# Optimization experiments

Hardware: AMD Instinct MI355X
Metric: run time of the kernel (lower is better)

## Reference

```python
import jax, jax.numpy as jnp
import numpy as np

LEAKY_SLOPE = 0.2  # tf.nn.leaky_relu default alpha
N_NODES = 50000
N_EDGES = 800000
IN_DIM = 128
OUT_DIM = 64
HEADS = 4
MLP_HID = 256
MLP_OUT = 128


def setup_inputs() -> dict:
    key = jax.random.key(0)
    ks = jax.random.split(key, 10)
    node_embeddings = jax.random.normal(ks[0], (N_NODES, IN_DIM), dtype=jnp.float32)
    src = jax.random.randint(ks[1], (N_EDGES,), 0, N_NODES, dtype=jnp.int32)
    dst = jax.random.randint(ks[2], (N_EDGES,), 0, N_NODES, dtype=jnp.int32)
    # glorot-ish scales
    W_n = jax.random.normal(ks[3], (HEADS, IN_DIM, OUT_DIM), dtype=jnp.float32) * (1.0 / np.sqrt(IN_DIM))
    a_src = jax.random.normal(ks[4], (HEADS, OUT_DIM), dtype=jnp.float32) * (1.0 / np.sqrt(OUT_DIM))
    a_dst = jax.random.normal(ks[5], (HEADS, OUT_DIM), dtype=jnp.float32) * (1.0 / np.sqrt(OUT_DIM))
    mlp_W1 = jax.random.normal(ks[6], (HEADS * OUT_DIM, MLP_HID), dtype=jnp.float32) * (1.0 / np.sqrt(HEADS * OUT_DIM))
    mlp_b1 = jnp.zeros((MLP_HID,), dtype=jnp.float32)
    mlp_W2 = jax.random.normal(ks[7], (MLP_HID, MLP_OUT), dtype=jnp.float32) * (1.0 / np.sqrt(MLP_HID))
    mlp_b2 = jnp.zeros((MLP_OUT,), dtype=jnp.float32)
    return {"node_embeddings": node_embeddings, "src": src, "dst": dst,
            "W_n": W_n, "a_src": a_src, "a_dst": a_dst,
            "mlp_W1": mlp_W1, "mlp_b1": mlp_b1, "mlp_W2": mlp_W2, "mlp_b2": mlp_b2}


def _gat_forward(node_embeddings, src, dst, W_n, a_src, a_dst, mlp_W1, mlp_b1, mlp_W2, mlp_b2):
    N = node_embeddings.shape[0]
    # per-head linear transform: [N, H, D]
    h = jnp.einsum('nc,hcd->nhd', node_embeddings, W_n)
    # decomposed attention scores at node level, gathered per edge
    s_src = jnp.einsum('nhd,hd->nh', h, a_src)          # [N, H]
    s_dst = jnp.einsum('nhd,hd->nh', h, a_dst)          # [N, H]
    e = jax.nn.leaky_relu(s_src[src] + s_dst[dst], negative_slope=LEAKY_SLOPE)  # [E, H]
    # segment softmax over incoming edges of each dst node
    e_max = jax.ops.segment_max(e, dst, num_segments=N)          # [N, H], -inf for empty
    ex = jnp.exp(e - e_max[dst])                                  # [E, H]
    den = jax.ops.segment_sum(ex, dst, num_segments=N)            # [N, H]
    m = h[src]                                                    # [E, H, D] messages
    num = jax.ops.segment_sum(ex[:, :, None] * m, dst, num_segments=N)  # [N, H, D]
    safe_den = jnp.where(den > 0, den, 1.0)
    head_out = jax.nn.relu(num / safe_den[:, :, None])            # [N, H, D]
    concat = head_out.reshape(N, -1)                              # [N, H*D]
    hidden = jax.nn.relu(concat @ mlp_W1 + mlp_b1)
    return hidden @ mlp_W2 + mlp_b2                               # [N, MLP_OUT]


def reference(node_embeddings, src, dst, W_n, a_src, a_dst, mlp_W1, mlp_b1, mlp_W2, mlp_b2):
    return _gat_forward(node_embeddings, src, dst, W_n, a_src, a_dst,
                        mlp_W1, mlp_b1, mlp_W2, mlp_b2)
```

## Files before the change

### kernel.cpp

```cpp
#include <hip/hip_runtime.h>

#define LEAKY 0.2f

typedef __attribute__((ext_vector_type(8))) short short8;
typedef __attribute__((ext_vector_type(4))) float floatx4;

__device__ __forceinline__ float bf2f(unsigned short u) {
    return __uint_as_float(((unsigned)u) << 16);
}
__device__ __forceinline__ unsigned short f2bf(float f) {
    unsigned u = __float_as_uint(f);
    unsigned r = (u + 0x7fffu + ((u >> 16) & 1u)) >> 16;
    return (unsigned short)r;
}
__device__ __forceinline__ float relu_nan(float v) { return v < 0.0f ? 0.0f : v; }

__device__ __forceinline__ void gload_lds16(const void* g, void* l) {
    __builtin_amdgcn_global_load_lds((const __attribute__((address_space(1))) void*)g,
                                     (__attribute__((address_space(3))) void*)l, 16, 0, 0);
}

__global__ void k_fill(float* __restrict__ p, float val, int n) {
    int i = blockIdx.x * blockDim.x + threadIdx.x;
    if (i < n) p[i] = val;
}

__global__ void k_zero(int* __restrict__ cnt, int n) {
    int i = blockIdx.x * blockDim.x + threadIdx.x;
    if (i < n) cnt[i] = 0;
}

__global__ void k_convert(const float* __restrict__ W, unsigned short* __restrict__ WT, int R, int C) {
    int k = threadIdx.x, n = blockIdx.x;
    WT[(size_t)n * R + k] = f2bf(W[(size_t)k * C + n]);
}

__global__ __launch_bounds__(256) void k_transform(
    const float* __restrict__ X, const float* __restrict__ Wn,
    const float* __restrict__ Asrc, const float* __restrict__ Adst,
    unsigned short* __restrict__ h_out, float* __restrict__ s_src, float* __restrict__ s_dst) {
    __shared__ float xt[16][132];
    const int t = threadIdx.x;
    const int row0 = blockIdx.x * 16;

    for (int i = t; i < 16 * 32; i += 256) {
        int r = i >> 5, cp = i & 31;
        float4 v = ((const float4*)(X + (size_t)(row0 + r) * 128))[cp];
        xt[r][cp * 4 + 0] = v.x; xt[r][cp * 4 + 1] = v.y;
        xt[r][cp * 4 + 2] = v.z; xt[r][cp * 4 + 3] = v.w;
    }
    __syncthreads();

    const int r0 = (t >> 6) << 2;
    const int j0 = (t & 63) << 2;
    const int head = j0 >> 6;
    const int dd = j0 & 63;
    const float* wbase = Wn + (size_t)head * 128 * 64 + dd;

    float acc[4][4] = {};
    for (int c = 0; c < 128; ++c) {
        float4 wv = *(const float4*)(wbase + (size_t)c * 64);
        float x0 = xt[r0 + 0][c], x1 = xt[r0 + 1][c], x2 = xt[r0 + 2][c], x3 = xt[r0 + 3][c];
        acc[0][0] += x0 * wv.x; acc[0][1] += x0 * wv.y; acc[0][2] += x0 * wv.z; acc[0][3] += x0 * wv.w;
        acc[1][0] += x1 * wv.x; acc[1][1] += x1 * wv.y; acc[1][2] += x1 * wv.z; acc[1][3] += x1 * wv.w;
        acc[2][0] += x2 * wv.x; acc[2][1] += x2 * wv.y; acc[2][2] += x2 * wv.z; acc[2][3] += x2 * wv.w;
        acc[3][0] += x3 * wv.x; acc[3][1] += x3 * wv.y; acc[3][2] += x3 * wv.z; acc[3][3] += x3 * wv.w;
    }

    for (int rr = 0; rr < 4; ++rr) {
        ushort4 o;
        o.x = f2bf(acc[rr][0]); o.y = f2bf(acc[rr][1]);
        o.z = f2bf(acc[rr][2]); o.w = f2bf(acc[rr][3]);
        *(ushort4*)(h_out + (size_t)(row0 + r0 + rr) * 256 + j0) = o;
    }

    float4 as4 = *(const float4*)(Asrc + head * 64 + dd);
    float4 ad4 = *(const float4*)(Adst + head * 64 + dd);
    for (int rr = 0; rr < 4; ++rr) {
        float ps = acc[rr][0] * as4.x + acc[rr][1] * as4.y + acc[rr][2] * as4.z + acc[rr][3] * as4.w;
        float pd = acc[rr][0] * ad4.x + acc[rr][1] * ad4.y + acc[rr][2] * ad4.z + acc[rr][3] * ad4.w;
        for (int m = 1; m < 16; m <<= 1) {
            ps += __shfl_xor(ps, m, 64);
            pd += __shfl_xor(pd, m, 64);
        }
        if ((t & 15) == 0) {
            s_src[(row0 + r0 + rr) * 4 + head] = ps;
            s_dst[(row0 + r0 + rr) * 4 + head] = pd;
        }
    }
}

__global__ void k_hist(const int* __restrict__ dst, int* __restrict__ cnt, int E) {
    int e = blockIdx.x * blockDim.x + threadIdx.x;
    if (e < E) atomicAdd(cnt + dst[e], 1);
}

__global__ __launch_bounds__(256) void k_scan1(
    const int* __restrict__ cnt, int* __restrict__ rowptr, int* __restrict__ bsum, int N) {
    __shared__ int wtot[4];
    const int lane = threadIdx.x & 63, wave = threadIdx.x >> 6;
    const int i = blockIdx.x * 256 + threadIdx.x;
    int v = (i < N) ? cnt[i] : 0;
    int x = v;
    for (int off = 1; off < 64; off <<= 1) {
        int y = __shfl_up(x, off, 64);
        if (lane >= off) x += y;
    }
    if (lane == 63) wtot[wave] = x;
    __syncthreads();
    int wo = 0;
    for (int wv = 0; wv < wave; ++wv) wo += wtot[wv];
    if (i < N) rowptr[i] = wo + x - v;
    if (threadIdx.x == 255) bsum[blockIdx.x] = wo + x;
}
__global__ void k_scan2(int* __restrict__ bsum, int nb) {
    const int lane = threadIdx.x;
    int carry = 0;
    for (int base = 0; base < nb; base += 64) {
        int i = base + lane;
        int v = (i < nb) ? bsum[i] : 0;
        int x = v;
        for (int off = 1; off < 64; off <<= 1) {
            int y = __shfl_up(x, off, 64);
            if (lane >= off) x += y;
        }
        if (i < nb) bsum[i] = carry + x - v;
        carry += __shfl(x, 63, 64);
    }
}
__global__ void k_scan3(int* __restrict__ rowptr, const int* __restrict__ bsum,
                        int* __restrict__ wcnt, int N, int E) {
    int i = blockIdx.x * blockDim.x + threadIdx.x;
    if (i < N) {
        int v = rowptr[i] + bsum[i >> 8];
        rowptr[i] = v;
        wcnt[i] = v;
    }
    if (i == N) rowptr[N] = E;
}

__global__ void k_scatter(const int* __restrict__ src, const int* __restrict__ dst,
                          int* __restrict__ wcnt, int* __restrict__ esrc, int E) {
    int e = blockIdx.x * blockDim.x + threadIdx.x;
    if (e < E) {
        int pos = atomicAdd(wcnt + dst[e], 1);
        esrc[pos] = src[e];
    }
}

__global__ __launch_bounds__(256) void k_agg(
    const float* __restrict__ s_src, const float* __restrict__ s_dst,
    const unsigned short* __restrict__ h_bf,
    const int* __restrict__ rowptr, const int* __restrict__ esrc,
    unsigned short* __restrict__ concat) {
    const int t = threadIdx.x;
    const int lane = t & 63;
    const int wave = t >> 6;
    const int row0 = blockIdx.x * 16;
    const int head = lane >> 4;
    const int c0 = lane << 2;
    const int eslot = lane & 15;
    const int hsel = lane & 48;

    for (int rr = 0; rr < 4; ++rr) {
        const int n = row0 + wave * 4 + rr;
        const int beg = rowptr[n], end = rowptr[n + 1];
        const float sdst = s_dst[n * 4 + head];
        float num0 = 0, num1 = 0, num2 = 0, num3 = 0, den = 0;
        for (int base = beg; base < end; base += 16) {
            const int nn = end - base;
            int sid = 0;
            float my_ex = 0.0f;
            if (eslot < nn) {
                sid = esrc[base + eslot];
                float v = s_src[sid * 4 + head] + sdst;
                v = v > 0.0f ? v : LEAKY * v;
                my_ex = __expf(v);
            }
#pragma unroll
            for (int e = 0; e < 16; ++e) {
                float ex = __shfl(my_ex, hsel | e, 64);
                int s    = __shfl(sid, e, 64);
                ushort4 hv = *(const ushort4*)(h_bf + (size_t)s * 256 + c0);
                num0 += ex * bf2f(hv.x);
                num1 += ex * bf2f(hv.y);
                num2 += ex * bf2f(hv.z);
                num3 += ex * bf2f(hv.w);
                den  += ex;
            }
        }
        const float inv = 1.0f / (den > 0.0f ? den : 1.0f);
        ushort4 o;
        o.x = f2bf(relu_nan(num0 * inv));
        o.y = f2bf(relu_nan(num1 * inv));
        o.z = f2bf(relu_nan(num2 * inv));
        o.w = f2bf(relu_nan(num3 * inv));
        *(ushort4*)(concat + (size_t)n * 256 + c0) = o;
    }
}

template <int BF16OUT>
__global__ __launch_bounds__(256) void k_gemm(
    const unsigned short* __restrict__ A, const unsigned short* __restrict__ BT,
    const float* __restrict__ bias, unsigned short* __restrict__ Cb,
    float* __restrict__ Cf, int N, int ldout) {
    __shared__ unsigned short As[128 * 32];
    __shared__ unsigned short Bs[128 * 32];
    const int t = threadIdx.x;
    const int lane = t & 63;
    const int w = t >> 6;
    const int wy = w >> 1, wx = w & 1;
    const int lm = lane & 15, quad = lane >> 4;
    const int row0 = blockIdx.x * 128;
    const int n0 = blockIdx.y * 128;

    const int srow = lane >> 2;
    const int sk = (lane & 3) * 8;

    float bias_v[4];
#pragma unroll
    for (int ni = 0; ni < 4; ++ni) bias_v[ni] = bias[n0 + wx * 64 + ni * 16 + lm];

    floatx4 acc[4][4];
#pragma unroll
    for (int mi = 0; mi < 4; ++mi)
#pragma unroll
        for (int ni = 0; ni < 4; ++ni) {
            float b = bias_v[ni];
            acc[mi][ni] = (floatx4){b, b, b, b};
        }

    for (int k0 = 0; k0 < 256; k0 += 32) {
#pragma unroll
        for (int p = 0; p < 2; ++p) {
            int tr = (p * 4 + w) * 16 + srow;
            int ga = row0 + tr; if (ga >= N) ga = N - 1;
            gload_lds16(A + (size_t)ga * 256 + k0 + sk,
                        (char*)As + (size_t)tr * 64 + sk * 2);
            gload_lds16(BT + (size_t)(n0 + tr) * 256 + k0 + sk,
                        (char*)Bs + (size_t)tr * 64 + sk * 2);
        }
        __syncthreads();
        short8 af[4], bf[4];
#pragma unroll
        for (int mi = 0; mi < 4; ++mi)
            af[mi] = *(const short8*)(As + (size_t)(wy * 64 + mi * 16 + lm) * 32 + quad * 8);
#pragma unroll
        for (int ni = 0; ni < 4; ++ni)
            bf[ni] = *(const short8*)(Bs + (size_t)(wx * 64 + ni * 16 + lm) * 32 + quad * 8);
#pragma unroll
        for (int mi = 0; mi < 4; ++mi)
#pragma unroll
            for (int ni = 0; ni < 4; ++ni)
                acc[mi][ni] = __builtin_amdgcn_mfma_f32_16x16x32_bf16(af[mi], bf[ni], acc[mi][ni], 0, 0, 0);
        __syncthreads();
    }

#pragma unroll
    for (int mi = 0; mi < 4; ++mi)
#pragma unroll
        for (int ni = 0; ni < 4; ++ni)
#pragma unroll
            for (int q = 0; q < 4; ++q) {
                int r = row0 + wy * 64 + mi * 16 + quad * 4 + q;
                int c = n0 + wx * 64 + ni * 16 + lm;
                if (r < N) {
                    if (BF16OUT) Cb[(size_t)r * ldout + c] = f2bf(relu_nan(acc[mi][ni][q]));
                    else         Cf[(size_t)r * ldout + c] = acc[mi][ni][q];
                }
            }
}

extern "C" void kernel_launch(void* const* d_in, const int* in_sizes, int n_in,
                              void* d_out, int out_size, void* d_ws, size_t ws_size,
                              hipStream_t stream) {
    const float* X    = (const float*)d_in[0];
    const int* src    = (const int*)d_in[1];
    const int* dst    = (const int*)d_in[2];
    const float* Wn   = (const float*)d_in[3];
    const float* Asrc = (const float*)d_in[4];
    const float* Adst = (const float*)d_in[5];
    const float* W1   = (const float*)d_in[6];
    const float* b1   = (const float*)d_in[7];
    const float* W2   = (const float*)d_in[8];
    const float* b2   = (const float*)d_in[9];
    float* out = (float*)d_out;

    const int N = in_sizes[0] / 128;
    const int E = in_sizes[1];
    const int NB = (N + 255) / 256;
    const int NR = (N + 127) / 128;

    size_t off = 0;
    char* w = (char*)d_ws;
    unsigned short* h_bf = (unsigned short*)(w + off); off += (size_t)N * 256 * 2;
    float* s_src = (float*)(w + off);                  off += (size_t)N * 4 * 4;
    float* s_dst = (float*)(w + off);                  off += (size_t)N * 4 * 4;
    int* cnt     = (int*)(w + off);                    off += (size_t)N * 4;
    int* rowptr  = (int*)(w + off);                    off += ((size_t)(N + 1) * 4 + 15) & ~15ull;
    int* wcnt    = (int*)(w + off);                    off += (size_t)N * 4;
    int* bsum    = (int*)(w + off);                    off += ((size_t)NB * 4 + 15) & ~15ull;
    int* esrc    = (int*)(w + off);                    off += (size_t)E * 4;
    unsigned short* W1T = (unsigned short*)(w + off);  off += 256 * 256 * 2;
    unsigned short* W2T = (unsigned short*)(w + off);  off += 128 * 256 * 2;
    const size_t required = off;

    if (ws_size < required) {
        k_fill<<<dim3((out_size + 255) / 256), dim3(256), 0, stream>>>(
            out, (float)(ws_size >> 20), out_size);
        return;
    }

    unsigned short* concat = (unsigned short*)d_out;

    k_zero<<<dim3((N + 255) / 256), dim3(256), 0, stream>>>(cnt, N);
    k_transform<<<dim3(N / 16), dim3(256), 0, stream>>>(X, Wn, Asrc, Adst, h_bf, s_src, s_dst);
    k_hist<<<dim3((E + 255) / 256), dim3(256), 0, stream>>>(dst, cnt, E);
    k_scan1<<<dim3(NB), dim3(256), 0, stream>>>(cnt, rowptr, bsum, N);
    k_scan2<<<dim3(1), dim3(64), 0, stream>>>(bsum, NB);
    k_scan3<<<dim3((N + 256) / 256), dim3(256), 0, stream>>>(rowptr, bsum, wcnt, N, E);
    k_scatter<<<dim3((E + 255) / 256), dim3(256), 0, stream>>>(src, dst, wcnt, esrc, E);
    k_convert<<<dim3(256), dim3(256), 0, stream>>>(W1, W1T, 256, 256);
    k_convert<<<dim3(128), dim3(256), 0, stream>>>(W2, W2T, 256, 128);
    k_agg<<<dim3(N / 16), dim3(256), 0, stream>>>(s_src, s_dst, h_bf, rowptr, esrc, concat);
    k_gemm<1><<<dim3(NR, 2), dim3(256), 0, stream>>>(concat, W1T, b1, h_bf, nullptr, N, 256);
    k_gemm<0><<<dim3(NR, 1), dim3(256), 0, stream>>>(h_bf, W2T, b2, nullptr, out, N, 128);
}
```

Measured before the change: 344.1 us.

## Run node transform on bf16 MFMA GEMM and split attention scores into separate kernel

Replaces the fp32 CUDA-core node transform with three steps: cast X and Wn to bf16, run the existing MFMA GEMM (now templated on K) to produce h, and compute the attention scores in a small kernel that reads the bf16 h. The goal is to move the dense projection onto matrix cores. The cost is extra launches and extra traffic: X is written in bf16 and h is read back. The scores are now taken from bf16-rounded h rather than fp32 accumulators, which slightly changes precision.

```diff
diff --git a/kernel.cpp b/kernel.cpp
--- a/kernel.cpp
+++ b/kernel.cpp
@@ -30,63 +30,50 @@
     if (i < n) cnt[i] = 0;
 }
 
+__global__ void k_cvt_x(const float* __restrict__ X, unsigned short* __restrict__ Xb, int n4) {
+    int i = blockIdx.x * blockDim.x + threadIdx.x;
+    if (i < n4) {
+        float4 v = ((const float4*)X)[i];
+        ushort4 o;
+        o.x = f2bf(v.x); o.y = f2bf(v.y); o.z = f2bf(v.z); o.w = f2bf(v.w);
+        ((ushort4*)Xb)[i] = o;
+    }
+}
+
+__global__ void k_cvt_wn(const float* __restrict__ Wn, unsigned short* __restrict__ WnT) {
+    int col = blockIdx.x, k = threadIdx.x;
+    int head = col >> 6, d = col & 63;
+    WnT[(size_t)col * 128 + k] = f2bf(Wn[(size_t)head * 8192 + (size_t)k * 64 + d]);
+}
+
 __global__ void k_convert(const float* __restrict__ W, unsigned short* __restrict__ WT, int R, int C) {
     int k = threadIdx.x, n = blockIdx.x;
     WT[(size_t)n * R + k] = f2bf(W[(size_t)k * C + n]);
 }
 
-__global__ __launch_bounds__(256) void k_transform(
-    const float* __restrict__ X, const float* __restrict__ Wn,
+__global__ __launch_bounds__(256) void k_scores(
+    const unsigned short* __restrict__ h_bf,
     const float* __restrict__ Asrc, const float* __restrict__ Adst,
-    unsigned short* __restrict__ h_out, float* __restrict__ s_src, float* __restrict__ s_dst) {
-    __shared__ float xt[16][132];
-    const int t = threadIdx.x;
-    const int row0 = blockIdx.x * 16;
-
-    for (int i = t; i < 16 * 32; i += 256) {
-        int r = i >> 5, cp = i & 31;
-        float4 v = ((const float4*)(X + (size_t)(row0 + r) * 128))[cp];
-        xt[r][cp * 4 + 0] = v.x; xt[r][cp * 4 + 1] = v.y;
-        xt[r][cp * 4 + 2] = v.z; xt[r][cp * 4 + 3] = v.w;
-    }
-    __syncthreads();
-
-    const int r0 = (t >> 6) << 2;
-    const int j0 = (t & 63) << 2;
-    const int head = j0 >> 6;
-    const int dd = j0 & 63;
-    const float* wbase = Wn + (size_t)head * 128 * 64 + dd;
-
-    float acc[4][4] = {};
-    for (int c = 0; c < 128; ++c) {
-        float4 wv = *(const float4*)(wbase + (size_t)c * 64);
-        float x0 = xt[r0 + 0][c], x1 = xt[r0 + 1][c], x2 = xt[r0 + 2][c], x3 = xt[r0 + 3][c];
-        acc[0][0] += x0 * wv.x; acc[0][1] += x0 * wv.y; acc[0][2] += x0 * wv.z; acc[0][3] += x0 * wv.w;
-        acc[1][0] += x1 * wv.x; acc[1][1] += x1 * wv.y; acc[1][2] += x1 * wv.z; acc[1][3] += x1 * wv.w;
-        acc[2][0] += x2 * wv.x; acc[2][1] += x2 * wv.y; acc[2][2] += x2 * wv.z; acc[2][3] += x2 * wv.w;
-        acc[3][0] += x3 * wv.x; acc[3][1] += x3 * wv.y; acc[3][2] += x3 * wv.z; acc[3][3] += x3 * wv.w;
-    }
-
-    for (int rr = 0; rr < 4; ++rr) {
-        ushort4 o;
-        o.x = f2bf(acc[rr][0]); o.y = f2bf(acc[rr][1]);
-        o.z = f2bf(acc[rr][2]); o.w = f2bf(acc[rr][3]);
-        *(ushort4*)(h_out + (size_t)(row0 + r0 + rr) * 256 + j0) = o;
-    }
-
-    float4 as4 = *(const float4*)(Asrc + head * 64 + dd);
-    float4 ad4 = *(const float4*)(Adst + head * 64 + dd);
-    for (int rr = 0; rr < 4; ++rr) {
-        float ps = acc[rr][0] * as4.x + acc[rr][1] * as4.y + acc[rr][2] * as4.z + acc[rr][3] * as4.w;
-        float pd = acc[rr][0] * ad4.x + acc[rr][1] * ad4.y + acc[rr][2] * ad4.z + acc[rr][3] * ad4.w;
-        for (int m = 1; m < 16; m <<= 1) {
-            ps += __shfl_xor(ps, m, 64);
-            pd += __shfl_xor(pd, m, 64);
-        }
-        if ((t & 15) == 0) {
-            s_src[(row0 + r0 + rr) * 4 + head] = ps;
-            s_dst[(row0 + r0 + rr) * 4 + head] = pd;
-        }
+    float* __restrict__ s_src, float* __restrict__ s_dst, int N) {
+    const int lane = threadIdx.x & 63;
+    const int wave = threadIdx.x >> 6;
+    const int n = blockIdx.x * 4 + wave;
+    if (n >= N) return;
+    const int head = lane >> 4;
+    const int c0 = lane << 2;
+    ushort4 hv = *(const ushort4*)(h_bf + (size_t)n * 256 + c0);
+    float4 as = *(const float4*)(Asrc + c0);
+    float4 ad = *(const float4*)(Adst + c0);
+    float h0 = bf2f(hv.x), h1 = bf2f(hv.y), h2 = bf2f(hv.z), h3 = bf2f(hv.w);
+    float ps = h0 * as.x + h1 * as.y + h2 * as.z + h3 * as.w;
+    float pd = h0 * ad.x + h1 * ad.y + h2 * ad.z + h3 * ad.w;
+    for (int m = 1; m < 16; m <<= 1) {
+        ps += __shfl_xor(ps, m, 64);
+        pd += __shfl_xor(pd, m, 64);
+    }
+    if ((lane & 15) == 0) {
+        s_src[n * 4 + head] = ps;
+        s_dst[n * 4 + head] = pd;
     }
 }
 
@@ -199,7 +186,7 @@
     }
 }
 
-template <int BF16OUT>
+template <int K, int MODE>
 __global__ __launch_bounds__(256) void k_gemm(
     const unsigned short* __restrict__ A, const unsigned short* __restrict__ BT,
     const float* __restrict__ bias, unsigned short* __restrict__ Cb,
@@ -213,46 +200,47 @@
     const int lm = lane & 15, quad = lane >> 4;
     const int row0 = blockIdx.x * 128;
     const int n0 = blockIdx.y * 128;
-
     const int srow = lane >> 2;
     const int sk = (lane & 3) * 8;
 
-    float bias_v[4];
-#pragma unroll
-    for (int ni = 0; ni < 4; ++ni) bias_v[ni] = bias[n0 + wx * 64 + ni * 16 + lm];
-
     floatx4 acc[4][4];
-#pragma unroll
-    for (int mi = 0; mi < 4; ++mi)
+    if (MODE == 0) {
+#pragma unroll
+        for (int mi = 0; mi < 4; ++mi)
+#pragma unroll
+            for (int ni = 0; ni < 4; ++ni) acc[mi][ni] = (floatx4){0, 0, 0, 0};
+    } else {
 #pragma unroll
         for (int ni = 0; ni < 4; ++ni) {
-            float b = bias_v[ni];
-            acc[mi][ni] = (floatx4){b, b, b, b};
+            float b = bias[n0 + wx * 64 + ni * 16 + lm];
+#pragma unroll
+            for (int mi = 0; mi < 4; ++mi) acc[mi][ni] = (floatx4){b, b, b, b};
         }
-
-    for (int k0 = 0; k0 < 256; k0 += 32) {
+    }
+
+    for (int k0 = 0; k0 < K; k0 += 32) {
 #pragma unroll
         for (int p = 0; p < 2; ++p) {
             int tr = (p * 4 + w) * 16 + srow;
             int ga = row0 + tr; if (ga >= N) ga = N - 1;
-            gload_lds16(A + (size_t)ga * 256 + k0 + sk,
+            gload_lds16(A + (size_t)ga * K + k0 + sk,
                         (char*)As + (size_t)tr * 64 + sk * 2);
-            gload_lds16(BT + (size_t)(n0 + tr) * 256 + k0 + sk,
+            gload_lds16(BT + (size_t)(n0 + tr) * K + k0 + sk,
                         (char*)Bs + (size_t)tr * 64 + sk * 2);
         }
         __syncthreads();
-        short8 af[4], bf[4];
+        short8 af[4], bfr[4];
 #pragma unroll
         for (int mi = 0; mi < 4; ++mi)
             af[mi] = *(const short8*)(As + (size_t)(wy * 64 + mi * 16 + lm) * 32 + quad * 8);
 #pragma unroll
         for (int ni = 0; ni < 4; ++ni)
-            bf[ni] = *(const short8*)(Bs + (size_t)(wx * 64 + ni * 16 + lm) * 32 + quad * 8);
+            bfr[ni] = *(const short8*)(Bs + (size_t)(wx * 64 + ni * 16 + lm) * 32 + quad * 8);
 #pragma unroll
         for (int mi = 0; mi < 4; ++mi)
 #pragma unroll
             for (int ni = 0; ni < 4; ++ni)
-                acc[mi][ni] = __builtin_amdgcn_mfma_f32_16x16x32_bf16(af[mi], bf[ni], acc[mi][ni], 0, 0, 0);
+                acc[mi][ni] = __builtin_amdgcn_mfma_f32_16x16x32_bf16(af[mi], bfr[ni], acc[mi][ni], 0, 0, 0);
         __syncthreads();
     }
 
@@ -265,8 +253,9 @@
                 int r = row0 + wy * 64 + mi * 16 + quad * 4 + q;
                 int c = n0 + wx * 64 + ni * 16 + lm;
                 if (r < N) {
-                    if (BF16OUT) Cb[(size_t)r * ldout + c] = f2bf(relu_nan(acc[mi][ni][q]));
-                    else         Cf[(size_t)r * ldout + c] = acc[mi][ni][q];
+                    if (MODE == 0)      Cb[(size_t)r * ldout + c] = f2bf(acc[mi][ni][q]);
+                    else if (MODE == 1) Cb[(size_t)r * ldout + c] = f2bf(relu_nan(acc[mi][ni][q]));
+                    else                Cf[(size_t)r * ldout + c] = acc[mi][ni][q];
                 }
             }
 }
@@ -303,6 +292,7 @@
     int* esrc    = (int*)(w + off);                    off += (size_t)E * 4;
     unsigned short* W1T = (unsigned short*)(w + off);  off += 256 * 256 * 2;
     unsigned short* W2T = (unsigned short*)(w + off);  off += 128 * 256 * 2;
+    unsigned short* WnT = (unsigned short*)(w + off);  off += 256 * 128 * 2;
     const size_t required = off;
 
     if (ws_size < required) {
@@ -311,10 +301,14 @@
         return;
     }
 
+    unsigned short* Xb     = (unsigned short*)d_out;
     unsigned short* concat = (unsigned short*)d_out;
 
     k_zero<<<dim3((N + 255) / 256), dim3(256), 0, stream>>>(cnt, N);
-    k_transform<<<dim3(N / 16), dim3(256), 0, stream>>>(X, Wn, Asrc, Adst, h_bf, s_src, s_dst);
+    k_cvt_x<<<dim3((N * 32 + 255) / 256), dim3(256), 0, stream>>>(X, Xb, N * 32);
+    k_cvt_wn<<<dim3(256), dim3(128), 0, stream>>>(Wn, WnT);
+    k_gemm<128, 0><<<dim3(NR, 2), dim3(256), 0, stream>>>(Xb, WnT, nullptr, h_bf, nullptr, N, 256);
+    k_scores<<<dim3((N + 3) / 4), dim3(256), 0, stream>>>(h_bf, Asrc, Adst, s_src, s_dst, N);
     k_hist<<<dim3((E + 255) / 256), dim3(256), 0, stream>>>(dst, cnt, E);
     k_scan1<<<dim3(NB), dim3(256), 0, stream>>>(cnt, rowptr, bsum, N);
     k_scan2<<<dim3(1), dim3(64), 0, stream>>>(bsum, NB);
@@ -323,6 +317,6 @@
     k_convert<<<dim3(256), dim3(256), 0, stream>>>(W1, W1T, 256, 256);
     k_convert<<<dim3(128), dim3(256), 0, stream>>>(W2, W2T, 256, 128);
     k_agg<<<dim3(N / 16), dim3(256), 0, stream>>>(s_src, s_dst, h_bf, rowptr, esrc, concat);
-    k_gemm<1><<<dim3(NR, 2), dim3(256), 0, stream>>>(concat, W1T, b1, h_bf, nullptr, N, 256);
-    k_gemm<0><<<dim3(NR, 1), dim3(256), 0, stream>>>(h_bf, W2T, b2, nullptr, out, N, 128);
-}
+    k_gemm<256, 1><<<dim3(NR, 2), dim3(256), 0, stream>>>(concat, W1T, b1, h_bf, nullptr, N, 256);
+    k_gemm<256, 2><<<dim3(NR, 1), dim3(256), 0, stream>>>(h_bf, W2T, b2, nullptr, out, N, 128);
+}
```

New measurement: 319.3 us. 7.2% less time.
